# Optimization experiments

Hardware: AMD Instinct MI355X
Metric: run time of the kernel (lower is better)

The kernel has to match this reference:

```python
import jax, jax.numpy as jnp
import numpy as np

N = 1048576        # batch
DTOT = 64          # total dims in u
D = 32             # transformed dims (len(nodes))
K = 40             # knots = num spline bins
B = 5.0            # tail bound: bins/2 = ceil(max|limit|)


def setup_inputs() -> dict:
    key = jax.random.key(0)
    k1, k2, k3, k4 = jax.random.split(key, 4)
    # scale inputs so they cover many bins and some fall in the identity tails
    u = jax.random.normal(k1, (N, DTOT), jnp.float32) * 3.0
    w = jax.random.uniform(k2, (D, K), jnp.float32, -0.5, 0.5)
    h = jax.random.uniform(k3, (D, K), jnp.float32, -0.5, 0.5)
    d = jax.random.uniform(k4, (D, K - 1), jnp.float32, -0.5, 0.5)
    nodes = jnp.arange(D, dtype=jnp.int32)
    return {"u": u, "w": w, "h": h, "d": d, "nodes": nodes}


def _rqs_forward(x, w, h, d):
    # x: [N, D] selected dims; w,h: [D, K]; d: [D, K-1]
    dt = x.dtype
    widths = jax.nn.softmax(w, axis=-1) * (2.0 * B)          # [D, K]
    cumw = jnp.concatenate(
        [jnp.full((D, 1), -B, dt), -B + jnp.cumsum(widths, -1)], -1)  # [D, K+1]
    heights = jax.nn.softmax(h, axis=-1) * (2.0 * B)
    cumh = jnp.concatenate(
        [jnp.full((D, 1), -B, dt), -B + jnp.cumsum(heights, -1)], -1)
    # interior derivatives via softplus, boundary derivatives fixed to 1 (linear tails)
    derivs = jnp.concatenate(
        [jnp.ones((D, 1), dt), jax.nn.softplus(d), jnp.ones((D, 1), dt)], -1)  # [D, K+1]

    inside = jnp.abs(x) <= B
    xc = jnp.clip(x, -B, B)
    # per-dim bin search (irregular, data-dependent)
    idx = jax.vmap(lambda kn, xd: jnp.searchsorted(kn, xd, side='right'))(cumw, xc.T).T - 1
    idx = jnp.clip(idx, 0, K - 1)                             # [N, D]

    dd = jnp.arange(D)[None, :]
    cw = cumw[dd, idx]; bw = widths[dd, idx]
    ch = cumh[dd, idx]; bh = heights[dd, idx]
    d0 = derivs[dd, idx]; d1 = derivs[dd, idx + 1]
    delta = bh / bw                                            # bin slope

    theta = (xc - cw) / bw
    t1m = theta * (1.0 - theta)
    denom = delta + (d0 + d1 - 2.0 * delta) * t1m
    num = bh * (delta * theta * theta + d0 * t1m)
    y = ch + num / denom
    logdet = (jnp.log(delta * delta * (d1 * theta * theta
                                       + 2.0 * delta * t1m
                                       + d0 * (1.0 - theta) ** 2))
              - 2.0 * jnp.log(denom))

    y = jnp.where(inside, y, x)                # identity tails
    logdet = jnp.where(inside, logdet, 0.0)
    return y, logdet.sum(-1)                   # [N, D], [N]


def reference(u, w, h, d, nodes):
    y, logd = _rqs_forward(u[:, nodes], w, h, d)
    x = u.at[:, nodes].set(y)
    return x, logd
```

## Files before the change

kernel.cpp:

```cpp
#include <hip/hip_runtime.h>
#include <math.h>

#define NROWS 1048576
#define DTOT  64
#define D     32
#define K     40
#define Bf    5.0f
#define G     128
#define GS    132
#define TP    (K + 1)

#define OFF_T1   0
#define OFF_DER  (D * TP * 16)
#define OFF_GS   (OFF_DER + D * TP * 4)
#define WS_BYTES (OFF_GS + D * G)

__global__ __launch_bounds__(64) void build_tables(
    const float* __restrict__ w, const float* __restrict__ h,
    const float* __restrict__ dk,
    float* __restrict__ der_g, float4* __restrict__ T1_g,
    unsigned char* __restrict__ gs_g)
{
    const int j = blockIdx.x;
    const int k = threadIdx.x;
    __shared__ float s_cumw[K + 1];

    float wv = (k < K) ? w[j * K + k] : -INFINITY;
    float hv = (k < K) ? h[j * K + k] : -INFINITY;
    float mw = wv, mh = hv;
    for (int m = 32; m > 0; m >>= 1) {
        mw = fmaxf(mw, __shfl_xor(mw, m));
        mh = fmaxf(mh, __shfl_xor(mh, m));
    }
    float ew = (k < K) ? __expf(wv - mw) : 0.f;
    float eh = (k < K) ? __expf(hv - mh) : 0.f;
    float sw = ew, sh = eh;
    for (int m = 32; m > 0; m >>= 1) {
        sw += __shfl_xor(sw, m);
        sh += __shfl_xor(sh, m);
    }
    float width  = ew / sw * (2.f * Bf);
    float height = eh / sh * (2.f * Bf);

    float iw = width, ih = height;
    for (int off = 1; off < 64; off <<= 1) {
        float a = __shfl_up(iw, off);
        float b = __shfl_up(ih, off);
        if (k >= off) { iw += a; ih += b; }
    }
    float cw_k = -Bf + (iw - width);
    float ch_k = -Bf + (ih - height);

    if (k <= K) {
        float dv = 1.f;
        if (k > 0 && k < K) dv = log1pf(__expf(dk[j * (K - 1) + (k - 1)]));
        der_g[j * TP + k] = dv;
    }
    if (k < K) {
        s_cumw[k] = cw_k;
        T1_g[j * TP + k] = make_float4(cw_k, 1.f / width, ch_k, height);
    }
    if (k == K - 1) s_cumw[K] = -Bf + iw;
    if (k == K) T1_g[j * TP + K] = make_float4(0.f, 0.f, 0.f, 0.f);

    __syncthreads();

    for (int c = k; c < G; c += 64) {
        float L = -Bf + (2.f * Bf) * ((float)c / (float)G);
        int idx = 0;
        for (int m = 1; m < K; ++m)
            if (s_cumw[m] <= L) idx = m;
        gs_g[j * G + c] = (unsigned char)idx;
    }
}

__global__ __launch_bounds__(256, 5) void rqs_main(
    const float4* __restrict__ u4,
    const float* __restrict__ der_g, const float4* __restrict__ T1_g,
    const unsigned char* __restrict__ gs_g,
    float4* __restrict__ x4, float* __restrict__ logd, int ntiles)
{
    __shared__ float4 s_T1[D * TP];
    __shared__ float  s_der[D * TP];
    __shared__ unsigned char s_gs[D * GS];

    const int t = threadIdx.x;
    for (int i = t; i < D * TP; i += 256) {
        s_T1[i]  = T1_g[i];
        s_der[i] = der_g[i];
    }
    for (int i = t; i < D * G; i += 256)
        s_gs[(i >> 7) * GS + (i & (G - 1))] = gs_g[i];
    __syncthreads();

    const int seg = t & 7;
    const int rl  = t >> 3;

    for (int tile = blockIdx.x; tile < ntiles; tile += gridDim.x) {
        const int row = tile * 32 + rl;

        const float4 vp = u4[row * 16 + 8 + seg];
        float4 v        = u4[row * 16 + seg];
        x4[row * 16 + 8 + seg] = vp;

        float vv[4] = {v.x, v.y, v.z, v.w};
        float ld = 0.f;
#pragma unroll
        for (int c = 0; c < 4; ++c) {
            const int j = seg * 4 + c;
            const float x = vv[c];
            const bool inside = fabsf(x) <= Bf;
            const float xc = fminf(fmaxf(x, -Bf), Bf);

            int cell = (int)((xc + Bf) * (G / (2.f * Bf)));
            cell = min(cell, G - 1);
            int i = s_gs[j * GS + cell];

            float4 tt = s_T1[j * TP + i];
            float theta = (xc - tt.x) * tt.y;
            while (theta >= 1.f && i < K - 1) {
                ++i;
                tt = s_T1[j * TP + i];
                theta = (xc - tt.x) * tt.y;
            }

            const float rbw = tt.y, ch = tt.z, bh = tt.w;
            const float d0 = s_der[j * TP + i];
            const float d1 = s_der[j * TP + i + 1];

            const float delta = bh * rbw;
            const float omt   = 1.f - theta;
            const float t1m   = theta * omt;
            const float th2   = theta * theta;
            const float denom = fmaf(fmaf(-2.f, delta, d0 + d1), t1m, delta);
            const float num   = bh * fmaf(d0, t1m, delta * th2);
            const float rd    = __builtin_amdgcn_rcpf(denom);
            const float y     = fmaf(num, rd, ch);
            const float Ap    = fmaf(d1, th2,
                                 fmaf(2.f * delta, t1m, d0 * omt * omt));
            const float ldet  = __logf(delta * delta * Ap * rd * rd);

            vv[c] = inside ? y : x;
            ld += inside ? ldet : 0.f;
        }
        x4[row * 16 + seg] = make_float4(vv[0], vv[1], vv[2], vv[3]);

        ld += __shfl_xor(ld, 1);
        ld += __shfl_xor(ld, 2);
        ld += __shfl_xor(ld, 4);
        if (seg == 0) logd[row] = ld;
    }
}

extern "C" void kernel_launch(void* const* d_in, const int* in_sizes, int n_in,
                              void* d_out, int out_size, void* d_ws, size_t ws_size,
                              hipStream_t stream) {
    const float* u  = (const float*)d_in[0];
    const float* w  = (const float*)d_in[1];
    const float* h  = (const float*)d_in[2];
    const float* dk = (const float*)d_in[3];

    float4* T1        = (float4*)d_ws;
    float*  der       = (float*)((char*)d_ws + OFF_DER);
    unsigned char* gs = (unsigned char*)d_ws + OFF_GS;

    float* xout = (float*)d_out;
    float* logd = (float*)d_out + (size_t)NROWS * DTOT;

    build_tables<<<D, 64, 0, stream>>>(w, h, dk, der, T1, gs);

    const int ntiles = NROWS / 32;
    rqs_main<<<1280, 256, 0, stream>>>((const float4*)u, der, T1, gs,
                                       (float4*)xout, logd, ntiles);
}
```

Measured before the change: 454.3 us.

## Restructure LUT tables, branchless bin select, product-log, prefetch next tile

Reorganizes the shared-memory tables into two float4 arrays, one holding the current and next bin edge/reciprocal width and one holding bin height and both derivatives. This replaces the data-dependent while loop with a single branchless advance-by-one and cuts the number of LDS loads. The log-determinant is now computed once per thread as the log of a product instead of four logs. The kernel also software-prefetches the next tile's input, and launch bounds and grid size change. The single-step advance assumes the coarse grid lookup is never more than one bin off. Multiplying terms before the log risks overflow or underflow.

```diff
diff --git a/kernel.cpp b/kernel.cpp
--- a/kernel.cpp
+++ b/kernel.cpp
@@ -10,16 +10,20 @@
 #define GS    132
 #define TP    (K + 1)
 
-#define OFF_T1   0
-#define OFF_DER  (D * TP * 16)
-#define OFF_GS   (OFF_DER + D * TP * 4)
-#define WS_BYTES (OFF_GS + D * G)
+#define OFF_CUMW 0
+#define OFF_DER  (D * (K + 1))
+#define OFF_RBW  (2 * D * (K + 1))
+#define OFF_CH   (2 * D * (K + 1) + D * K)
+#define OFF_BH   (2 * D * (K + 1) + 2 * D * K)
+#define OFF_GS_BYTES ((2 * D * (K + 1) + 3 * D * K) * 4)
+#define WS_BYTES (OFF_GS_BYTES + D * G)
 
 __global__ __launch_bounds__(64) void build_tables(
     const float* __restrict__ w, const float* __restrict__ h,
     const float* __restrict__ dk,
-    float* __restrict__ der_g, float4* __restrict__ T1_g,
-    unsigned char* __restrict__ gs_g)
+    float* __restrict__ cumw_g, float* __restrict__ der_g,
+    float* __restrict__ rbw_g, float* __restrict__ ch_g,
+    float* __restrict__ bh_g, unsigned char* __restrict__ gs_g)
 {
     const int j = blockIdx.x;
     const int k = threadIdx.x;
@@ -48,21 +52,26 @@
         float b = __shfl_up(ih, off);
         if (k >= off) { iw += a; ih += b; }
     }
-    float cw_k = -Bf + (iw - width);
-    float ch_k = -Bf + (ih - height);
+    const float cw_k    = -Bf + (iw - width);
+    const float ch_k    = -Bf + (ih - height);
+    const float cw_next = -Bf + iw;
 
     if (k <= K) {
         float dv = 1.f;
         if (k > 0 && k < K) dv = log1pf(__expf(dk[j * (K - 1) + (k - 1)]));
-        der_g[j * TP + k] = dv;
+        der_g[j * (K + 1) + k] = dv;
     }
     if (k < K) {
+        cumw_g[j * (K + 1) + k] = cw_k;
+        rbw_g[j * K + k] = 1.f / width;
+        ch_g [j * K + k] = ch_k;
+        bh_g [j * K + k] = height;
         s_cumw[k] = cw_k;
-        T1_g[j * TP + k] = make_float4(cw_k, 1.f / width, ch_k, height);
-    }
-    if (k == K - 1) s_cumw[K] = -Bf + iw;
-    if (k == K) T1_g[j * TP + K] = make_float4(0.f, 0.f, 0.f, 0.f);
-
+    }
+    if (k == K - 1) {
+        cumw_g[j * (K + 1) + K] = cw_next;
+        s_cumw[K] = cw_next;
+    }
     __syncthreads();
 
     for (int c = k; c < G; c += 64) {
@@ -74,37 +83,62 @@
     }
 }
 
-__global__ __launch_bounds__(256, 5) void rqs_main(
+__global__ __launch_bounds__(256, 3) void rqs_main(
     const float4* __restrict__ u4,
-    const float* __restrict__ der_g, const float4* __restrict__ T1_g,
-    const unsigned char* __restrict__ gs_g,
+    const float* __restrict__ cumw_g, const float* __restrict__ der_g,
+    const float* __restrict__ rbw_g, const float* __restrict__ ch_g,
+    const float* __restrict__ bh_g, const unsigned char* __restrict__ gs_g,
     float4* __restrict__ x4, float* __restrict__ logd, int ntiles)
 {
-    __shared__ float4 s_T1[D * TP];
-    __shared__ float  s_der[D * TP];
+    __shared__ float4 s_sel[D * TP];
+    __shared__ float4 s_bin[D * TP];
     __shared__ unsigned char s_gs[D * GS];
 
     const int t = threadIdx.x;
-    for (int i = t; i < D * TP; i += 256) {
-        s_T1[i]  = T1_g[i];
-        s_der[i] = der_g[i];
-    }
-    for (int i = t; i < D * G; i += 256)
-        s_gs[(i >> 7) * GS + (i & (G - 1))] = gs_g[i];
+    for (int e = t; e < D * K; e += 256) {
+        const int j = e / K, k = e - j * K;
+        const float cw0 = cumw_g[j * (K + 1) + k];
+        const float cw1 = cumw_g[j * (K + 1) + k + 1];
+        const float rb0 = rbw_g[e];
+        const float rb1 = (k < K - 1) ? rbw_g[e + 1] : 1.f;
+        s_sel[j * TP + k] = make_float4(cw0, rb0, cw1, rb1);
+        s_bin[j * TP + k] = make_float4(ch_g[e], bh_g[e],
+                                        der_g[j * (K + 1) + k],
+                                        der_g[j * (K + 1) + k + 1]);
+    }
+    for (int i = t; i < D * G / 4; i += 256) {
+        const int r = i >> 5, wi = i & 31;
+        *(uint32_t*)(s_gs + r * GS + wi * 4) = ((const uint32_t*)gs_g)[i];
+    }
     __syncthreads();
 
     const int seg = t & 7;
     const int rl  = t >> 3;
 
-    for (int tile = blockIdx.x; tile < ntiles; tile += gridDim.x) {
+    int tile = blockIdx.x;
+    float4 vt = make_float4(0.f, 0.f, 0.f, 0.f);
+    float4 vp = make_float4(0.f, 0.f, 0.f, 0.f);
+    if (tile < ntiles) {
         const int row = tile * 32 + rl;
-
-        const float4 vp = u4[row * 16 + 8 + seg];
-        float4 v        = u4[row * 16 + seg];
+        vt = u4[row * 16 + seg];
+        vp = u4[row * 16 + 8 + seg];
+    }
+
+    for (; tile < ntiles; tile += gridDim.x) {
+        const int next = tile + gridDim.x;
+        float4 nt = make_float4(0.f, 0.f, 0.f, 0.f);
+        float4 np = make_float4(0.f, 0.f, 0.f, 0.f);
+        if (next < ntiles) {
+            const int nrow = next * 32 + rl;
+            nt = u4[nrow * 16 + seg];
+            np = u4[nrow * 16 + 8 + seg];
+        }
+
+        const int row = tile * 32 + rl;
         x4[row * 16 + 8 + seg] = vp;
 
-        float vv[4] = {v.x, v.y, v.z, v.w};
-        float ld = 0.f;
+        float vv[4] = {vt.x, vt.y, vt.z, vt.w};
+        float prod = 1.f;
 #pragma unroll
         for (int c = 0; c < 4; ++c) {
             const int j = seg * 4 + c;
@@ -116,19 +150,17 @@
             cell = min(cell, G - 1);
             int i = s_gs[j * GS + cell];
 
-            float4 tt = s_T1[j * TP + i];
-            float theta = (xc - tt.x) * tt.y;
-            while (theta >= 1.f && i < K - 1) {
-                ++i;
-                tt = s_T1[j * TP + i];
-                theta = (xc - tt.x) * tt.y;
-            }
-
-            const float rbw = tt.y, ch = tt.z, bh = tt.w;
-            const float d0 = s_der[j * TP + i];
-            const float d1 = s_der[j * TP + i + 1];
+            const float4 s = s_sel[j * TP + i];
+            const bool adv = (xc >= s.z) && (i < K - 1);
+            const float cw  = adv ? s.z : s.x;
+            const float rbw = adv ? s.w : s.y;
+            i += adv;
+
+            const float4 b = s_bin[j * TP + i];
+            const float ch = b.x, bh = b.y, d0 = b.z, d1 = b.w;
 
             const float delta = bh * rbw;
+            const float theta = (xc - cw) * rbw;
             const float omt   = 1.f - theta;
             const float t1m   = theta * omt;
             const float th2   = theta * theta;
@@ -138,17 +170,20 @@
             const float y     = fmaf(num, rd, ch);
             const float Ap    = fmaf(d1, th2,
                                  fmaf(2.f * delta, t1m, d0 * omt * omt));
-            const float ldet  = __logf(delta * delta * Ap * rd * rd);
+            const float term  = delta * delta * Ap * (rd * rd);
 
             vv[c] = inside ? y : x;
-            ld += inside ? ldet : 0.f;
+            prod  = inside ? prod * term : prod;
         }
         x4[row * 16 + seg] = make_float4(vv[0], vv[1], vv[2], vv[3]);
 
+        float ld = __logf(prod);
         ld += __shfl_xor(ld, 1);
         ld += __shfl_xor(ld, 2);
         ld += __shfl_xor(ld, 4);
         if (seg == 0) logd[row] = ld;
+
+        vt = nt; vp = np;
     }
 }
 
@@ -160,16 +195,20 @@
     const float* h  = (const float*)d_in[2];
     const float* dk = (const float*)d_in[3];
 
-    float4* T1        = (float4*)d_ws;
-    float*  der       = (float*)((char*)d_ws + OFF_DER);
-    unsigned char* gs = (unsigned char*)d_ws + OFF_GS;
+    float* ws   = (float*)d_ws;
+    float* cumw = ws + OFF_CUMW;
+    float* der  = ws + OFF_DER;
+    float* rbw  = ws + OFF_RBW;
+    float* ch   = ws + OFF_CH;
+    float* bh   = ws + OFF_BH;
+    unsigned char* gs = (unsigned char*)d_ws + OFF_GS_BYTES;
 
     float* xout = (float*)d_out;
     float* logd = (float*)d_out + (size_t)NROWS * DTOT;
 
-    build_tables<<<D, 64, 0, stream>>>(w, h, dk, der, T1, gs);
+    build_tables<<<D, 64, 0, stream>>>(w, h, dk, cumw, der, rbw, ch, bh, gs);
 
     const int ntiles = NROWS / 32;
-    rqs_main<<<1280, 256, 0, stream>>>((const float4*)u, der, T1, gs,
-                                       (float4*)xout, logd, ntiles);
+    rqs_main<<<1536, 256, 0, stream>>>((const float4*)u, cumw, der, rbw, ch, bh,
+                                       gs, (float4*)xout, logd, ntiles);
 }
```

Result: no change. 454.8 us (+0.1%).
